# Kernel optimization log

Hardware: AMD Instinct MI355X
Metric: run time of the kernel (lower is better)

The kernel has to match this reference:

```python
import jax, jax.numpy as jnp
import numpy as np

# Dims fixed by ExpertC.__init__ defaults
INPUT_DIM, HIDDEN, OUT_DIM, NLAYERS = 1024, 256, 256, 2
D_STATE, EXPAND, HEADDIM = 32, 2, 32
D_INNER = EXPAND * HIDDEN                      # 512
NHEADS = D_INNER // HEADDIM                    # 16
CONV_DIM = D_INNER + 2 * D_STATE               # 576 (x, B, C; ngroups=1)
D_IN_PROJ = 2 * D_INNER + 2 * D_STATE + NHEADS # 1104 (z, xBC, dt)
KCONV = 4
B, L = 16, 2048
EPS = 1e-5


def setup_inputs() -> dict:
    key = jax.random.key(0)
    ks = iter(jax.random.split(key, 40))
    rn = lambda shape, s: jax.random.normal(next(ks), shape, jnp.float32) * s
    inp = {}
    inp["x"] = rn((B, L, INPUT_DIM), 1.0)
    inp["ip_w"] = rn((INPUT_DIM, HIDDEN), INPUT_DIM ** -0.5)
    inp["ip_b"] = jnp.zeros((HIDDEN,), jnp.float32)
    inp["m_inw"] = rn((NLAYERS, HIDDEN, D_IN_PROJ), HIDDEN ** -0.5)
    inp["m_inb"] = jnp.zeros((NLAYERS, D_IN_PROJ), jnp.float32)
    inp["m_convw"] = rn((NLAYERS, CONV_DIM, KCONV), 0.3)
    inp["m_convb"] = jnp.zeros((NLAYERS, CONV_DIM), jnp.float32)
    inp["m_dtb"] = rn((NLAYERS, NHEADS), 0.5)
    inp["m_Alog"] = jnp.log(1.0 + 15.0 * jax.random.uniform(next(ks), (NLAYERS, NHEADS), jnp.float32))
    inp["m_D"] = jnp.ones((NLAYERS, NHEADS), jnp.float32)
    inp["m_nw"] = jnp.ones((NLAYERS, D_INNER), jnp.float32)
    inp["m_outw"] = rn((NLAYERS, D_INNER, HIDDEN), D_INNER ** -0.5)
    inp["m_outb"] = jnp.zeros((NLAYERS, HIDDEN), jnp.float32)
    inp["rms_w"] = jnp.ones((NLAYERS, HIDDEN), jnp.float32)
    inp["ln1_w"] = jnp.ones((HIDDEN,), jnp.float32)
    inp["ln1_b"] = jnp.zeros((HIDDEN,), jnp.float32)
    inp["w1"] = rn((HIDDEN, 2 * HIDDEN), HIDDEN ** -0.5)
    inp["b1"] = jnp.zeros((2 * HIDDEN,), jnp.float32)
    inp["w2"] = rn((2 * HIDDEN, OUT_DIM), (2 * HIDDEN) ** -0.5)
    inp["b2"] = jnp.zeros((OUT_DIM,), jnp.float32)
    inp["ln2_w"] = jnp.ones((OUT_DIM,), jnp.float32)
    inp["ln2_b"] = jnp.zeros((OUT_DIM,), jnp.float32)
    return inp


def rmsnorm(x, w):
    return x * jax.lax.rsqrt(jnp.mean(x * x, axis=-1, keepdims=True) + EPS) * w


def layernorm(x, w, b):
    m = jnp.mean(x, axis=-1, keepdims=True)
    v = jnp.mean((x - m) ** 2, axis=-1, keepdims=True)
    return (x - m) * jax.lax.rsqrt(v + EPS) * w + b


def mamba_layer(x, inw, inb, convw, convb, dtb, Alog, D, nw, outw, outb):
    b, l, _ = x.shape
    zxbcdt = x @ inw + inb                                   # (b,l,1104)
    z, xBC, dt = jnp.split(zxbcdt, [D_INNER, D_INNER + CONV_DIM], axis=-1)
    dt = jax.nn.softplus(dt + dtb)                           # (b,l,h)
    # causal depthwise conv1d (kernel 4) + silu
    xp = jnp.pad(xBC, ((0, 0), (KCONV - 1, 0), (0, 0)))
    xBC = sum(xp[:, i:i + l, :] * convw[:, i] for i in range(KCONV)) + convb
    xBC = jax.nn.silu(xBC)
    xs, Bm, Cm = jnp.split(xBC, [D_INNER, D_INNER + D_STATE], axis=-1)
    xh = xs.reshape(b, l, NHEADS, HEADDIM)                   # (b,l,h,p)
    A = -jnp.exp(Alog)                                       # (h,)
    dA = jnp.exp(dt * A)                                     # (b,l,h)
    dtx = dt[..., None] * xh                                 # (b,l,h,p)

    def step(h, inp):
        dA_t, dtx_t, B_t, C_t = inp
        # h: (b,h,p,n)
        h = h * dA_t[:, :, None, None] + dtx_t[..., None] * B_t[:, None, None, :]
        y = jnp.einsum('bhpn,bn->bhp', h, C_t)
        return h, y

    h0 = jnp.zeros((b, NHEADS, HEADDIM, D_STATE), x.dtype)
    xs_t = (jnp.moveaxis(dA, 1, 0), jnp.moveaxis(dtx, 1, 0),
            jnp.moveaxis(Bm, 1, 0), jnp.moveaxis(Cm, 1, 0))
    _, ys = jax.lax.scan(step, h0, xs_t)                     # (l,b,h,p)
    y = jnp.moveaxis(ys, 0, 1) + D[None, None, :, None] * xh
    y = y.reshape(b, l, D_INNER)
    y = rmsnorm(y * jax.nn.silu(z), nw)                      # gated RMSNorm
    return y @ outw + outb


def _expert(x, ip_w, ip_b, m_inw, m_inb, m_convw, m_convb, m_dtb, m_Alog, m_D,
            m_nw, m_outw, m_outb, rms_w, ln1_w, ln1_b, w1, b1, w2, b2, ln2_w, ln2_b):
    if x.ndim == 2:
        x = x[:, None, :]
    x = x @ ip_w + ip_b
    for i in range(NLAYERS):
        res = x
        x = mamba_layer(x, m_inw[i], m_inb[i], m_convw[i], m_convb[i], m_dtb[i],
                        m_Alog[i], m_D[i], m_nw[i], m_outw[i], m_outb[i])
        x = rmsnorm(x + res, rms_w[i])
    x = layernorm(x, ln1_w, ln1_b)
    x = jax.nn.gelu(x @ w1 + b1, approximate=False)          # dropout is eval no-op
    x = x @ w2 + b2
    return layernorm(x, ln2_w, ln2_b)


def reference(x, ip_w, ip_b, m_inw, m_inb, m_convw, m_convb, m_dtb, m_Alog, m_D,
              m_nw, m_outw, m_outb, rms_w, ln1_w, ln1_b, w1, b1, w2, b2, ln2_w, ln2_b):
    return _expert(x, ip_w, ip_b, m_inw, m_inb, m_convw, m_convb, m_dtb, m_Alog, m_D,
                   m_nw, m_outw, m_outb, rms_w, ln1_w, ln1_b, w1, b1, w2, b2, ln2_w, ln2_b)
```

## Files before the change

kernel.cpp:

```cpp
#include <hip/hip_runtime.h>

typedef __bf16 bf16;
typedef __bf16 bf16x8 __attribute__((ext_vector_type(8)));
typedef float  f32x4  __attribute__((ext_vector_type(4)));

#define EPSF 1e-5f

__device__ __forceinline__ float bf2f(bf16 x) { return (float)x; }
__device__ __forceinline__ bf16  f2bf(float x) { return (bf16)x; }
__device__ __forceinline__ float siluf(float x) { return x / (1.f + expf(-x)); }

struct PrepackArgs {
    const float* W[7];
    bf16* TH[7];
    bf16* TL[7];
    int K[7];
    int N[7];
};

__global__ __launch_bounds__(256) void prepack_kernel(PrepackArgs a)
{
    int s = blockIdx.y;
    int idx = blockIdx.x * 256 + threadIdx.x;
    int K = a.K[s], N = a.N[s];
    if (idx >= K * N) return;
    int k = idx / N, n = idx - k * N;
    float v = a.W[s][idx];
    bf16 hi = f2bf(v);
    a.TH[s][(size_t)n * K + k] = hi;
    a.TL[s][(size_t)n * K + k] = f2bf(v - bf2f(hi));
}

__global__ __launch_bounds__(256) void gemm_hl(
    const bf16* __restrict__ AH, const bf16* __restrict__ AL,
    const float* __restrict__ Af, int lda,
    const bf16* __restrict__ WTh, const bf16* __restrict__ WTl,
    const float* __restrict__ bias,
    int N, int K,
    float* __restrict__ outF, int ldF,
    bf16* __restrict__ outB, int ldB,
    bf16* __restrict__ outH, bf16* __restrict__ outL, int ldH,
    int doGelu,
    const float* __restrict__ dtb, const float* __restrict__ Alog,
    float* __restrict__ dtf, float* __restrict__ dAf)
{
    __shared__ bf16 As [128][40];
    __shared__ bf16 Als[128][40];

    const int tid  = threadIdx.x;
    const int lane = tid & 63;
    const int wid  = tid >> 6;
    const int waveM = wid & 1, waveN = wid >> 1;
    const int m16 = lane & 15, quad = lane >> 4;
    const int row0 = blockIdx.x * 128;
    const int n0   = blockIdx.y * 64;

    f32x4 acc[4][2];
#pragma unroll
    for (int i = 0; i < 4; ++i)
#pragma unroll
        for (int j = 0; j < 2; ++j)
            acc[i][j] = (f32x4){0.f, 0.f, 0.f, 0.f};

    const int ar = tid >> 1, akc = (tid & 1) * 16;

    const int bn0 = min(n0 + waveN * 32 + m16,      N - 1);
    const int bn1 = min(n0 + waveN * 32 + 16 + m16, N - 1);
    const bf16* bH0p = WTh + (size_t)bn0 * K + quad * 8;
    const bf16* bH1p = WTh + (size_t)bn1 * K + quad * 8;
    const bf16* bL0p = WTl + (size_t)bn0 * K + quad * 8;
    const bf16* bL1p = WTl + (size_t)bn1 * K + quad * 8;

    bf16x8 bH[2], bL[2], bHn[2], bLn[2];
    bH[0] = *(const bf16x8*)(bH0p);
    bH[1] = *(const bf16x8*)(bH1p);
    bL[0] = *(const bf16x8*)(bL0p);
    bL[1] = *(const bf16x8*)(bL1p);

    for (int k0 = 0; k0 < K; k0 += 32) {
        if (AH) {
            const bf16* s0 = AH + (size_t)(row0 + ar) * lda + k0 + akc;
            const bf16* s1 = AL + (size_t)(row0 + ar) * lda + k0 + akc;
            *(uint4*)&As [ar][akc]     = *(const uint4*)s0;
            *(uint4*)&As [ar][akc + 8] = *(const uint4*)(s0 + 8);
            *(uint4*)&Als[ar][akc]     = *(const uint4*)s1;
            *(uint4*)&Als[ar][akc + 8] = *(const uint4*)(s1 + 8);
        } else {
            const float* asrc = Af + (size_t)(row0 + ar) * lda + k0 + akc;
            float f[16];
            *(float4*)&f[0]  = ((const float4*)asrc)[0];
            *(float4*)&f[4]  = ((const float4*)asrc)[1];
            *(float4*)&f[8]  = ((const float4*)asrc)[2];
            *(float4*)&f[12] = ((const float4*)asrc)[3];
            bf16 hv[16], lv[16];
#pragma unroll
            for (int c = 0; c < 16; ++c) {
                bf16 hi = f2bf(f[c]);
                hv[c] = hi;
                lv[c] = f2bf(f[c] - bf2f(hi));
            }
            *(uint4*)&As [ar][akc]     = *(uint4*)&hv[0];
            *(uint4*)&As [ar][akc + 8] = *(uint4*)&hv[8];
            *(uint4*)&Als[ar][akc]     = *(uint4*)&lv[0];
            *(uint4*)&Als[ar][akc + 8] = *(uint4*)&lv[8];
        }
        __syncthreads();

        const bool more = (k0 + 32) < K;
        if (more) {
            int kn = k0 + 32;
            bHn[0] = *(const bf16x8*)(bH0p + kn);
            bHn[1] = *(const bf16x8*)(bH1p + kn);
            bLn[0] = *(const bf16x8*)(bL0p + kn);
            bLn[1] = *(const bf16x8*)(bL1p + kn);
        }

        bf16x8 aH[4], aL[4];
#pragma unroll
        for (int mi = 0; mi < 4; ++mi) {
            aH[mi] = *(const bf16x8*)&As [waveM * 64 + mi * 16 + m16][quad * 8];
            aL[mi] = *(const bf16x8*)&Als[waveM * 64 + mi * 16 + m16][quad * 8];
        }

#pragma unroll
        for (int mi = 0; mi < 4; ++mi)
#pragma unroll
            for (int ni = 0; ni < 2; ++ni) {
                acc[mi][ni] = __builtin_amdgcn_mfma_f32_16x16x32_bf16(
                    aH[mi], bH[ni], acc[mi][ni], 0, 0, 0);
                acc[mi][ni] = __builtin_amdgcn_mfma_f32_16x16x32_bf16(
                    aH[mi], bL[ni], acc[mi][ni], 0, 0, 0);
                acc[mi][ni] = __builtin_amdgcn_mfma_f32_16x16x32_bf16(
                    aL[mi], bH[ni], acc[mi][ni], 0, 0, 0);
            }
        __syncthreads();

        if (more) {
            bH[0] = bHn[0]; bH[1] = bHn[1];
            bL[0] = bLn[0]; bL[1] = bLn[1];
        }
    }

#pragma unroll
    for (int ni = 0; ni < 2; ++ni) {
        int col = n0 + waveN * 32 + ni * 16 + m16;
        if (col >= N) continue;
        float bv = bias ? bias[col] : 0.f;
#pragma unroll
        for (int mi = 0; mi < 4; ++mi) {
#pragma unroll
            for (int r = 0; r < 4; ++r) {
                int row = row0 + waveM * 64 + mi * 16 + quad * 4 + r;
                float v = acc[mi][ni][r] + bv;
                if (dtf && col >= 1088) {
                    int head = col - 1088;
                    float xx = v + dtb[head];
                    float sp = (xx > 20.f) ? xx : log1pf(expf(xx));
                    float A  = -expf(Alog[head]);
                    dtf[(size_t)row * 16 + head] = sp;
                    dAf[(size_t)row * 16 + head] = expf(sp * A);
                } else {
                    if (doGelu) v = 0.5f * v * (1.f + erff(v * 0.70710678118654752f));
                    if (outB) outB[(size_t)row * ldB + col] = f2bf(v);
                    if (outF) outF[(size_t)row * ldF + col] = v;
                    if (outH) {
                        bf16 hi = f2bf(v);
                        outH[(size_t)row * ldH + col] = hi;
                        outL[(size_t)row * ldH + col] = f2bf(v - bf2f(hi));
                    }
                }
            }
        }
    }
}

__global__ __launch_bounds__(256) void conv_kernel(
    const bf16* __restrict__ zx,
    const float* __restrict__ cw,
    const float* __restrict__ cbias,
    float* __restrict__ xs,
    float* __restrict__ Bc,
    float* __restrict__ Cc)
{
    int g = blockIdx.x * 256 + threadIdx.x;
    if (g >= 32768 * 72) return;
    int row = g / 72;
    int cb8 = g - row * 72;
    int ch  = cb8 * 8;
    int l   = row & 2047;

    float4 wv[8];
#pragma unroll
    for (int c = 0; c < 8; ++c)
        wv[c] = *(const float4*)(cw + (ch + c) * 4);

    float acc[8];
    {
        float4 b0 = *(const float4*)(cbias + ch);
        float4 b1 = *(const float4*)(cbias + ch + 4);
        acc[0] = b0.x; acc[1] = b0.y; acc[2] = b0.z; acc[3] = b0.w;
        acc[4] = b1.x; acc[5] = b1.y; acc[6] = b1.z; acc[7] = b1.w;
    }

#pragma unroll
    for (int i = 0; i < 4; ++i) {
        int ls = l + i - 3;
        if (ls >= 0) {
            bf16x8 v = *(const bf16x8*)(zx + (size_t)(row + i - 3) * 1104 + 512 + ch);
#pragma unroll
            for (int c = 0; c < 8; ++c)
                acc[c] = fmaf(bf2f(v[c]), (&wv[c].x)[i], acc[c]);
        }
    }

    float s[8];
#pragma unroll
    for (int c = 0; c < 8; ++c) s[c] = siluf(acc[c]);

    if (cb8 < 64) {
        float* dst = xs + (size_t)row * 512 + ch;
        ((float4*)dst)[0] = (float4){s[0], s[1], s[2], s[3]};
        ((float4*)dst)[1] = (float4){s[4], s[5], s[6], s[7]};
    } else if (cb8 < 68) {
        float* dst = Bc + (size_t)row * 32 + (ch - 512);
        ((float4*)dst)[0] = (float4){s[0], s[1], s[2], s[3]};
        ((float4*)dst)[1] = (float4){s[4], s[5], s[6], s[7]};
    } else {
        float* dst = Cc + (size_t)row * 32 + (ch - 544);
        ((float4*)dst)[0] = (float4){s[0], s[1], s[2], s[3]};
        ((float4*)dst)[1] = (float4){s[4], s[5], s[6], s[7]};
    }
}

#define QCH   64
#define NCH   32

struct StepB  { float Bv[16]; float da, dtv, xv; };
struct StepBC { float Bv[16]; float Cv[16]; float da, dtv, xv; };

__device__ __forceinline__ void load_stepB(
    StepB& S, const float* Bc, const float* dtf, const float* dAf,
    const float* xs, size_t r, int h, int p, int nb)
{
    const float4* bp = (const float4*)(Bc + r * 32 + nb);
    *(float4*)&S.Bv[0]  = bp[0];
    *(float4*)&S.Bv[4]  = bp[1];
    *(float4*)&S.Bv[8]  = bp[2];
    *(float4*)&S.Bv[12] = bp[3];
    S.da  = dAf[r * 16 + h];
    S.dtv = dtf[r * 16 + h];
    S.xv  = xs[r * 512 + h * 32 + p];
}

__device__ __forceinline__ void load_stepBC(
    StepBC& S, const float* Bc, const float* Cc, const float* dtf,
    const float* dAf, const float* xs, size_t r, int h, int p, int nb)
{
    const float4* bp = (const float4*)(Bc + r * 32 + nb);
    *(float4*)&S.Bv[0]  = bp[0];
    *(float4*)&S.Bv[4]  = bp[1];
    *(float4*)&S.Bv[8]  = bp[2];
    *(float4*)&S.Bv[12] = bp[3];
    const float4* cp = (const float4*)(Cc + r * 32 + nb);
    *(float4*)&S.Cv[0]  = cp[0];
    *(float4*)&S.Cv[4]  = cp[1];
    *(float4*)&S.Cv[8]  = cp[2];
    *(float4*)&S.Cv[12] = cp[3];
    S.da  = dAf[r * 16 + h];
    S.dtv = dtf[r * 16 + h];
    S.xv  = xs[r * 512 + h * 32 + p];
}

__global__ __launch_bounds__(256) void scan_phase1(
    const float* __restrict__ xs,
    const float* __restrict__ Bc,
    const float* __restrict__ dtf,
    const float* __restrict__ dAf,
    float* __restrict__ cs,
    float* __restrict__ cp)
{
    int blk = blockIdx.x * 4 + (threadIdx.x >> 6);
    int bh = blk >> 5, c = blk & (NCH - 1);
    int b = bh >> 4, h = bh & 15;
    int lane = threadIdx.x & 63;
    int p = lane & 31, half = lane >> 5, nb = half * 16;
    float hs[16];
#pragma unroll
    for (int j = 0; j < 16; ++j) hs[j] = 0.f;
    float P = 1.f;
    size_t rb = (size_t)b * 2048 + (size_t)c * QCH;

    StepB S0, S1;
    load_stepB(S0, Bc, dtf, dAf, xs, rb, h, p, nb);

    for (int t = 0; t < QCH; t += 2) {
        load_stepB(S1, Bc, dtf, dAf, xs, rb + t + 1, h, p, nb);
        {
            float dtx = S0.dtv * S0.xv, da = S0.da;
#pragma unroll
            for (int j = 0; j < 16; ++j)
                hs[j] = fmaf(hs[j], da, dtx * S0.Bv[j]);
            P *= da;
        }
        if (t + 2 < QCH)
            load_stepB(S0, Bc, dtf, dAf, xs, rb + t + 2, h, p, nb);
        {
            float dtx = S1.dtv * S1.xv, da = S1.da;
#pragma unroll
            for (int j = 0; j < 16; ++j)
                hs[j] = fmaf(hs[j], da, dtx * S1.Bv[j]);
            P *= da;
        }
    }

    float* dst = cs + (size_t)blk * 1024 + lane * 16;
#pragma unroll
    for (int q = 0; q < 4; ++q)
        ((float4*)dst)[q] = (float4){hs[q*4], hs[q*4+1], hs[q*4+2], hs[q*4+3]};
    if (lane == 0) cp[blk] = P;
}

__global__ __launch_bounds__(64) void scan_phase2(
    float* __restrict__ cs,
    const float* __restrict__ cp)
{
    int bh = blockIdx.x;
    int lane = threadIdx.x;
    float H[16];
#pragma unroll
    for (int j = 0; j < 16; ++j) H[j] = 0.f;
    for (int c = 0; c < NCH; ++c) {
        float* base = cs + ((size_t)(bh * NCH + c)) * 1024 + lane * 16;
        float E[16];
#pragma unroll
        for (int q = 0; q < 4; ++q) {
            float4 v = ((const float4*)base)[q];
            E[q*4] = v.x; E[q*4+1] = v.y; E[q*4+2] = v.z; E[q*4+3] = v.w;
        }
        float P = cp[bh * NCH + c];
#pragma unroll
        for (int q = 0; q < 4; ++q)
            ((float4*)base)[q] = (float4){H[q*4], H[q*4+1], H[q*4+2], H[q*4+3]};
#pragma unroll
        for (int j = 0; j < 16; ++j)
            H[j] = fmaf(H[j], P, E[j]);
    }
}

__global__ __launch_bounds__(256) void scan_phase3(
    const float* __restrict__ xs,
    const float* __restrict__ Bc,
    const float* __restrict__ Cc,
    const float* __restrict__ dtf,
    const float* __restrict__ dAf,
    const float* __restrict__ Dv,
    const float* __restrict__ cs,
    bf16* __restrict__ zx)
{
    int blk = blockIdx.x * 4 + (threadIdx.x >> 6);
    int bh = blk >> 5, c = blk & (NCH - 1);
    int b = bh >> 4, h = bh & 15;
    int lane = threadIdx.x & 63;
    int p = lane & 31, half = lane >> 5, nb = half * 16;
    float Dh = Dv[h];
    float hs[16];
    {
        const float* src = cs + (size_t)blk * 1024 + lane * 16;
#pragma unroll
        for (int q = 0; q < 4; ++q) {
            float4 v = ((const float4*)src)[q];
            hs[q*4] = v.x; hs[q*4+1] = v.y; hs[q*4+2] = v.z; hs[q*4+3] = v.w;
        }
    }
    size_t rb = (size_t)b * 2048 + (size_t)c * QCH;

    StepBC S0, S1;
    load_stepBC(S0, Bc, Cc, dtf, dAf, xs, rb, h, p, nb);

    for (int t = 0; t < QCH; t += 2) {
        load_stepBC(S1, Bc, Cc, dtf, dAf, xs, rb + t + 1, h, p, nb);
        {
            float dtx = S0.dtv * S0.xv, da = S0.da;
            float y0 = 0.f, y1 = 0.f, y2 = 0.f, y3 = 0.f;
#pragma unroll
            for (int j = 0; j < 16; j += 4) {
                hs[j]   = fmaf(hs[j],   da, dtx * S0.Bv[j]);   y0 = fmaf(hs[j],   S0.Cv[j],   y0);
                hs[j+1] = fmaf(hs[j+1], da, dtx * S0.Bv[j+1]); y1 = fmaf(hs[j+1], S0.Cv[j+1], y1);
                hs[j+2] = fmaf(hs[j+2], da, dtx * S0.Bv[j+2]); y2 = fmaf(hs[j+2], S0.Cv[j+2], y2);
                hs[j+3] = fmaf(hs[j+3], da, dtx * S0.Bv[j+3]); y3 = fmaf(hs[j+3], S0.Cv[j+3], y3);
            }
            float yv = (y0 + y1) + (y2 + y3);
            yv += __shfl_xor(yv, 32);
            if (half == 0)
                zx[(rb + t) * 1104 + 512 + h * 32 + p] = f2bf(yv + Dh * S0.xv);
        }
        if (t + 2 < QCH)
            load_stepBC(S0, Bc, Cc, dtf, dAf, xs, rb + t + 2, h, p, nb);
        {
            float dtx = S1.dtv * S1.xv, da = S1.da;
            float y0 = 0.f, y1 = 0.f, y2 = 0.f, y3 = 0.f;
#pragma unroll
            for (int j = 0; j < 16; j += 4) {
                hs[j]   = fmaf(hs[j],   da, dtx * S1.Bv[j]);   y0 = fmaf(hs[j],   S1.Cv[j],   y0);
                hs[j+1] = fmaf(hs[j+1], da, dtx * S1.Bv[j+1]); y1 = fmaf(hs[j+1], S1.Cv[j+1], y1);
                hs[j+2] = fmaf(hs[j+2], da, dtx * S1.Bv[j+2]); y2 = fmaf(hs[j+2], S1.Cv[j+2], y2);
                hs[j+3] = fmaf(hs[j+3], da, dtx * S1.Bv[j+3]); y3 = fmaf(hs[j+3], S1.Cv[j+3], y3);
            }
            float yv = (y0 + y1) + (y2 + y3);
            yv += __shfl_xor(yv, 32);
            if (half == 0)
                zx[(rb + t + 1) * 1104 + 512 + h * 32 + p] = f2bf(yv + Dh * S1.xv);
        }
    }
}

__global__ __launch_bounds__(256) void gaterms_kernel(
    const bf16* __restrict__ zx,
    const float* __restrict__ nw,
    bf16* __restrict__ outH,
    bf16* __restrict__ outL)
{
    int row = blockIdx.x * 4 + (threadIdx.x >> 6);
    int lane = threadIdx.x & 63;
    union { uint4 u; bf16 b[8]; } yv, zv, oh, ol;
    yv.u = *(const uint4*)(zx + (size_t)row * 1104 + 512 + lane * 8);
    zv.u = *(const uint4*)(zx + (size_t)row * 1104 + lane * 8);
    float4 nv0 = *(const float4*)(nw + lane * 8);
    float4 nv1 = *(const float4*)(nw + lane * 8 + 4);
    float nvv[8] = {nv0.x, nv0.y, nv0.z, nv0.w, nv1.x, nv1.y, nv1.z, nv1.w};
    float g[8]; float ss = 0.f;
#pragma unroll
    for (int i = 0; i < 8; ++i) {
        float gate = siluf(bf2f(zv.b[i]));
        g[i] = bf2f(yv.b[i]) * gate;
        ss += g[i] * g[i];
    }
#pragma unroll
    for (int o = 1; o < 64; o <<= 1) ss += __shfl_xor(ss, o);
    float rms = rsqrtf(ss * (1.f / 512.f) + EPSF);
#pragma unroll
    for (int i = 0; i < 8; ++i) {
        float v = g[i] * rms * nvv[i];
        bf16 hi = f2bf(v);
        oh.b[i] = hi;
        ol.b[i] = f2bf(v - bf2f(hi));
    }
    *(uint4*)(outH + (size_t)row * 512 + lane * 8) = oh.u;
    *(uint4*)(outL + (size_t)row * 512 + lane * 8) = ol.u;
}

__global__ __launch_bounds__(256) void resrms_kernel(
    const float* __restrict__ mo,
    float* __restrict__ h,
    const float* __restrict__ w,
    bf16* __restrict__ oH,
    bf16* __restrict__ oL)
{
    int row = blockIdx.x * 4 + (threadIdx.x >> 6);
    int lane = threadIdx.x & 63;
    float4 a = *(const float4*)(mo + (size_t)row * 256 + lane * 4);
    float4 r = *(const float4*)(h  + (size_t)row * 256 + lane * 4);
    float s0 = a.x + r.x, s1 = a.y + r.y, s2 = a.z + r.z, s3 = a.w + r.w;
    float ss = s0 * s0 + s1 * s1 + s2 * s2 + s3 * s3;
#pragma unroll
    for (int o = 1; o < 64; o <<= 1) ss += __shfl_xor(ss, o);
    float rms = rsqrtf(ss * (1.f / 256.f) + EPSF);
    float4 wv = *(const float4*)(w + lane * 4);
    float o0 = s0 * rms * wv.x, o1 = s1 * rms * wv.y;
    float o2 = s2 * rms * wv.z, o3 = s3 * rms * wv.w;
    *(float4*)(h + (size_t)row * 256 + lane * 4) = (float4){o0, o1, o2, o3};
    union { uint2 u; bf16 bb[4]; } uh, ul;
    float o[4] = {o0, o1, o2, o3};
#pragma unroll
    for (int i = 0; i < 4; ++i) {
        bf16 hi = f2bf(o[i]);
        uh.bb[i] = hi;
        ul.bb[i] = f2bf(o[i] - bf2f(hi));
    }
    *(uint2*)(oH + (size_t)row * 256 + lane * 4) = uh.u;
    *(uint2*)(oL + (size_t)row * 256 + lane * 4) = ul.u;
}

__global__ __launch_bounds__(256) void ln_kernel(
    const float* __restrict__ x,
    const float* __restrict__ w,
    const float* __restrict__ b,
    bf16* __restrict__ outH,
    bf16* __restrict__ outL,
    float* __restrict__ outF)
{
    int row = blockIdx.x * 4 + (threadIdx.x >> 6);
    int lane = threadIdx.x & 63;
    float4 v = *(const float4*)(x + (size_t)row * 256 + lane * 4);
    float sum = v.x + v.y + v.z + v.w;
    float sq  = v.x * v.x + v.y * v.y + v.z * v.z + v.w * v.w;
#pragma unroll
    for (int o = 1; o < 64; o <<= 1) { sum += __shfl_xor(sum, o); sq += __shfl_xor(sq, o); }
    float m  = sum * (1.f / 256.f);
    float var = sq * (1.f / 256.f) - m * m;
    float is = rsqrtf(var + EPSF);
    float4 wv = *(const float4*)(w + lane * 4);
    float4 bv = *(const float4*)(b + lane * 4);
    float o0 = (v.x - m) * is * wv.x + bv.x;
    float o1 = (v.y - m) * is * wv.y + bv.y;
    float o2 = (v.z - m) * is * wv.z + bv.z;
    float o3 = (v.w - m) * is * wv.w + bv.w;
    if (outH) {
        union { uint2 u; bf16 bb[4]; } oh, ol;
        float o[4] = {o0, o1, o2, o3};
#pragma unroll
        for (int i = 0; i < 4; ++i) {
            bf16 hi = f2bf(o[i]);
            oh.bb[i] = hi;
            ol.bb[i] = f2bf(o[i] - bf2f(hi));
        }
        *(uint2*)(outH + (size_t)row * 256 + lane * 4) = oh.u;
        *(uint2*)(outL + (size_t)row * 256 + lane * 4) = ol.u;
    }
    if (outF)
        *(float4*)(outF + (size_t)row * 256 + lane * 4) = (float4){o0, o1, o2, o3};
}

extern "C" void kernel_launch(void* const* d_in, const int* in_sizes, int n_in,
                              void* d_out, int out_size, void* d_ws, size_t ws_size,
                              hipStream_t stream)
{
    const float* x      = (const float*)d_in[0];
    const float* ip_w   = (const float*)d_in[1];
    const float* ip_b   = (const float*)d_in[2];
    const float* m_inw  = (const float*)d_in[3];
    const float* m_inb  = (const float*)d_in[4];
    const float* m_convw= (const float*)d_in[5];
    const float* m_convb= (const float*)d_in[6];
    const float* m_dtb  = (const float*)d_in[7];
    const float* m_Alog = (const float*)d_in[8];
    const float* m_D    = (const float*)d_in[9];
    const float* m_nw   = (const float*)d_in[10];
    const float* m_outw = (const float*)d_in[11];
    const float* m_outb = (const float*)d_in[12];
    const float* rms_w  = (const float*)d_in[13];
    const float* ln1_w  = (const float*)d_in[14];
    const float* ln1_b  = (const float*)d_in[15];
    const float* w1     = (const float*)d_in[16];
    const float* b1     = (const float*)d_in[17];
    const float* w2     = (const float*)d_in[18];
    const float* b2     = (const float*)d_in[19];
    const float* ln2_w  = (const float*)d_in[20];
    const float* ln2_b  = (const float*)d_in[21];

    const int M = 32768;
    char* wsb = (char*)d_ws;
    size_t off = 0;
    auto alloc = [&](size_t bytes) {
        void* p = wsb + off;
        off += (bytes + 255) & ~(size_t)255;
        return p;
    };
    bf16*  zx   = (bf16*) alloc((size_t)M * 1104 * 2);
    float* h    = (float*)alloc((size_t)M * 256 * 4);
    float* U1   = (float*)alloc((size_t)M * 512 * 4);
    float* Bc   = (float*)alloc((size_t)M * 32 * 4);
    float* Cc   = (float*)alloc((size_t)M * 32 * 4);
    float* dtf  = (float*)alloc((size_t)M * 16 * 4);
    float* dAf  = (float*)alloc((size_t)M * 16 * 4);
    float* cs   = (float*)alloc((size_t)8192 * 1024 * 4);
    float* cpb  = (float*)alloc((size_t)8192 * 4);
    bf16* ipTH   = (bf16*)alloc(262144 * 2);
    bf16* ipTL   = (bf16*)alloc(262144 * 2);
    bf16* inwTH0 = (bf16*)alloc(282624 * 2);
    bf16* inwTL0 = (bf16*)alloc(282624 * 2);
    bf16* inwTH1 = (bf16*)alloc(282624 * 2);
    bf16* inwTL1 = (bf16*)alloc(282624 * 2);
    bf16* outwTH0= (bf16*)alloc(131072 * 2);
    bf16* outwTL0= (bf16*)alloc(131072 * 2);
    bf16* outwTH1= (bf16*)alloc(131072 * 2);
    bf16* outwTL1= (bf16*)alloc(131072 * 2);
    bf16* w1TH   = (bf16*)alloc(131072 * 2);
    bf16* w1TL   = (bf16*)alloc(131072 * 2);
    bf16* w2TH   = (bf16*)alloc(131072 * 2);
    bf16* w2TL   = (bf16*)alloc(131072 * 2);
    (void)ws_size; (void)in_sizes; (void)n_in; (void)out_size;

    float* xs      = U1;
    bf16*  hH      = (bf16*)U1;
    bf16*  hL      = hH + (size_t)M * 256;
    bf16*  normedH = (bf16*)U1;
    bf16*  normedL = normedH + (size_t)M * 512;
    bf16*  tbH     = (bf16*)U1;
    bf16*  tbL     = tbH + (size_t)M * 256;
    float* mo      = (float*)zx;
    bf16*  gH      = (bf16*)zx;
    bf16*  gL      = gH + (size_t)M * 512;
    float* ubuf    = (float*)cs;

    PrepackArgs pa;
    pa.W[0] = ip_w;               pa.TH[0] = ipTH;    pa.TL[0] = ipTL;    pa.K[0] = 1024; pa.N[0] = 256;
    pa.W[1] = m_inw;              pa.TH[1] = inwTH0;  pa.TL[1] = inwTL0;  pa.K[1] = 256;  pa.N[1] = 1104;
    pa.W[2] = m_inw + 256*1104;   pa.TH[2] = inwTH1;  pa.TL[2] = inwTL1;  pa.K[2] = 256;  pa.N[2] = 1104;
    pa.W[3] = m_outw;             pa.TH[3] = outwTH0; pa.TL[3] = outwTL0; pa.K[3] = 512;  pa.N[3] = 256;
    pa.W[4] = m_outw + 512*256;   pa.TH[4] = outwTH1; pa.TL[4] = outwTL1; pa.K[4] = 512;  pa.N[4] = 256;
    pa.W[5] = w1;                 pa.TH[5] = w1TH;    pa.TL[5] = w1TL;    pa.K[5] = 256;  pa.N[5] = 512;
    pa.W[6] = w2;                 pa.TH[6] = w2TH;    pa.TL[6] = w2TL;    pa.K[6] = 512;  pa.N[6] = 256;
    prepack_kernel<<<dim3(1104, 7), 256, 0, stream>>>(pa);

    dim3 blk(256);

    gemm_hl<<<dim3(256, 4), blk, 0, stream>>>(
        nullptr, nullptr, x, 1024, ipTH, ipTL, ip_b, 256, 1024,
        h, 256, nullptr, 0, hH, hL, 256, 0,
        nullptr, nullptr, nullptr, nullptr);

    for (int L = 0; L < 2; ++L) {
        const bf16* inwTH = L ? inwTH1 : inwTH0;
        const bf16* inwTL = L ? inwTL1 : inwTL0;
        const bf16* outwTH= L ? outwTH1 : outwTH0;
        const bf16* outwTL= L ? outwTL1 : outwTL0;
        const float* inb = m_inb  + (size_t)L * 1104;
        const float* cw  = m_convw+ (size_t)L * 576 * 4;
        const float* cb  = m_convb+ (size_t)L * 576;
        const float* dtb = m_dtb  + L * 16;
        const float* Al  = m_Alog + L * 16;
        const float* Dv  = m_D    + L * 16;
        const float* nw  = m_nw   + (size_t)L * 512;
        const float* ob  = m_outb + (size_t)L * 256;
        const float* rw  = rms_w  + (size_t)L * 256;

        gemm_hl<<<dim3(256, 18), blk, 0, stream>>>(
            hH, hL, nullptr, 256, inwTH, inwTL, inb, 1104, 256,
            nullptr, 0, zx, 1104, nullptr, nullptr, 0, 0,
            dtb, Al, dtf, dAf);
        conv_kernel<<<9216, 256, 0, stream>>>(zx, cw, cb, xs, Bc, Cc);
        scan_phase1<<<2048, 256, 0, stream>>>(xs, Bc, dtf, dAf, cs, cpb);
        scan_phase2<<<256, 64, 0, stream>>>(cs, cpb);
        scan_phase3<<<2048, 256, 0, stream>>>(xs, Bc, Cc, dtf, dAf, Dv, cs, zx);
        gaterms_kernel<<<M / 4, 256, 0, stream>>>(zx, nw, normedH, normedL);
        gemm_hl<<<dim3(256, 4), blk, 0, stream>>>(
            normedH, normedL, nullptr, 512, outwTH, outwTL, ob, 256, 512,
            mo, 256, nullptr, 0, nullptr, nullptr, 0, 0,
            nullptr, nullptr, nullptr, nullptr);
        resrms_kernel<<<M / 4, 256, 0, stream>>>(mo, h, rw, hH, hL);
    }

    ln_kernel<<<M / 4, 256, 0, stream>>>(h, ln1_w, ln1_b, tbH, tbL, nullptr);
    gemm_hl<<<dim3(256, 8), blk, 0, stream>>>(
        tbH, tbL, nullptr, 256, w1TH, w1TL, b1, 512, 256,
        nullptr, 0, nullptr, 0, gH, gL, 512, 1,
        nullptr, nullptr, nullptr, nullptr);
    gemm_hl<<<dim3(256, 4), blk, 0, stream>>>(
        gH, gL, nullptr, 512, w2TH, w2TL, b2, 256, 512,
        ubuf, 256, nullptr, 0, nullptr, nullptr, 0, 0,
        nullptr, nullptr, nullptr, nullptr);
    ln_kernel<<<M / 4, 256, 0, stream>>>(ubuf, ln2_w, ln2_b, nullptr, nullptr, (float*)d_out);
}
```

Measured before the change: 1.564 ms.

## Double-buffer A tile in LDS with XOR swizzle and register prefetch

The GEMM A-tile staging now uses two LDS buffers. The next k-slice is loaded from global into registers before the MFMA loop and written to the alternate buffer afterwards, so each iteration needs one barrier instead of two. The hi and lo halves are packed into a single 64-wide row with an XOR swizzle to avoid LDS bank conflicts. This adds register pressure for the prefetched values and doubles LDS use per block, which may lower occupancy.

```diff
diff --git a/kernel.cpp b/kernel.cpp
--- a/kernel.cpp
+++ b/kernel.cpp
@@ -44,8 +44,7 @@
     const float* __restrict__ dtb, const float* __restrict__ Alog,
     float* __restrict__ dtf, float* __restrict__ dAf)
 {
-    __shared__ bf16 As [128][40];
-    __shared__ bf16 Als[128][40];
+    __shared__ bf16 As[2][128][64];
 
     const int tid  = threadIdx.x;
     const int lane = tid & 63;
@@ -62,7 +61,18 @@
         for (int j = 0; j < 2; ++j)
             acc[i][j] = (f32x4){0.f, 0.f, 0.f, 0.f};
 
-    const int ar = tid >> 1, akc = (tid & 1) * 16;
+    const int ar  = tid >> 1;
+    const int akc = (tid & 1) * 16;
+    const int ac0 = (tid & 1) * 2;
+    const int sw  = ar & 7;
+    const int sH0 = ((ac0 + 0) ^ sw) * 8;
+    const int sH1 = ((ac0 + 1) ^ sw) * 8;
+    const int sL0 = ((ac0 + 4) ^ sw) * 8;
+    const int sL1 = ((ac0 + 5) ^ sw) * 8;
+
+    const int rs = m16 & 7;
+    const int rH = ((quad + 0) ^ rs) * 8;
+    const int rL = ((quad + 4) ^ rs) * 8;
 
     const int bn0 = min(n0 + waveN * 32 + m16,      N - 1);
     const int bn1 = min(n0 + waveN * 32 + 16 + m16, N - 1);
@@ -77,21 +87,38 @@
     bL[0] = *(const bf16x8*)(bL0p);
     bL[1] = *(const bf16x8*)(bL1p);
 
-    for (int k0 = 0; k0 < K; k0 += 32) {
+    uint4  pH0, pH1, pL0, pL1;
+    float4 fA0, fA1, fA2, fA3;
+
+    auto loadA = [&](int k0) {
         if (AH) {
             const bf16* s0 = AH + (size_t)(row0 + ar) * lda + k0 + akc;
             const bf16* s1 = AL + (size_t)(row0 + ar) * lda + k0 + akc;
-            *(uint4*)&As [ar][akc]     = *(const uint4*)s0;
-            *(uint4*)&As [ar][akc + 8] = *(const uint4*)(s0 + 8);
-            *(uint4*)&Als[ar][akc]     = *(const uint4*)s1;
-            *(uint4*)&Als[ar][akc + 8] = *(const uint4*)(s1 + 8);
+            pH0 = *(const uint4*)s0;
+            pH1 = *(const uint4*)(s0 + 8);
+            pL0 = *(const uint4*)s1;
+            pL1 = *(const uint4*)(s1 + 8);
         } else {
             const float* asrc = Af + (size_t)(row0 + ar) * lda + k0 + akc;
+            fA0 = ((const float4*)asrc)[0];
+            fA1 = ((const float4*)asrc)[1];
+            fA2 = ((const float4*)asrc)[2];
+            fA3 = ((const float4*)asrc)[3];
+        }
+    };
+    auto writeA = [&](int buf) {
+        bf16* dst = &As[buf][ar][0];
+        if (AH) {
+            *(uint4*)(dst + sH0) = pH0;
+            *(uint4*)(dst + sH1) = pH1;
+            *(uint4*)(dst + sL0) = pL0;
+            *(uint4*)(dst + sL1) = pL1;
+        } else {
             float f[16];
-            *(float4*)&f[0]  = ((const float4*)asrc)[0];
-            *(float4*)&f[4]  = ((const float4*)asrc)[1];
-            *(float4*)&f[8]  = ((const float4*)asrc)[2];
-            *(float4*)&f[12] = ((const float4*)asrc)[3];
+            *(float4*)&f[0]  = fA0;
+            *(float4*)&f[4]  = fA1;
+            *(float4*)&f[8]  = fA2;
+            *(float4*)&f[12] = fA3;
             bf16 hv[16], lv[16];
 #pragma unroll
             for (int c = 0; c < 16; ++c) {
@@ -99,15 +126,23 @@
                 hv[c] = hi;
                 lv[c] = f2bf(f[c] - bf2f(hi));
             }
-            *(uint4*)&As [ar][akc]     = *(uint4*)&hv[0];
-            *(uint4*)&As [ar][akc + 8] = *(uint4*)&hv[8];
-            *(uint4*)&Als[ar][akc]     = *(uint4*)&lv[0];
-            *(uint4*)&Als[ar][akc + 8] = *(uint4*)&lv[8];
-        }
-        __syncthreads();
-
+            *(uint4*)(dst + sH0) = *(uint4*)&hv[0];
+            *(uint4*)(dst + sH1) = *(uint4*)&hv[8];
+            *(uint4*)(dst + sL0) = *(uint4*)&lv[0];
+            *(uint4*)(dst + sL1) = *(uint4*)&lv[8];
+        }
+    };
+
+    loadA(0);
+    writeA(0);
+    __syncthreads();
+
+    int cur = 0;
+    for (int k0 = 0; k0 < K; k0 += 32) {
         const bool more = (k0 + 32) < K;
+
         if (more) {
+            loadA(k0 + 32);
             int kn = k0 + 32;
             bHn[0] = *(const bf16x8*)(bH0p + kn);
             bHn[1] = *(const bf16x8*)(bH1p + kn);
@@ -118,8 +153,9 @@
         bf16x8 aH[4], aL[4];
 #pragma unroll
         for (int mi = 0; mi < 4; ++mi) {
-            aH[mi] = *(const bf16x8*)&As [waveM * 64 + mi * 16 + m16][quad * 8];
-            aL[mi] = *(const bf16x8*)&Als[waveM * 64 + mi * 16 + m16][quad * 8];
+            const bf16* base = &As[cur][waveM * 64 + mi * 16 + m16][0];
+            aH[mi] = *(const bf16x8*)(base + rH);
+            aL[mi] = *(const bf16x8*)(base + rL);
         }
 
 #pragma unroll
@@ -133,12 +169,14 @@
                 acc[mi][ni] = __builtin_amdgcn_mfma_f32_16x16x32_bf16(
                     aL[mi], bH[ni], acc[mi][ni], 0, 0, 0);
             }
+
+        if (more) writeA(cur ^ 1);
         __syncthreads();
-
         if (more) {
             bH[0] = bHn[0]; bH[1] = bHn[1];
             bL[0] = bLn[0]; bL[1] = bLn[1];
         }
+        cur ^= 1;
     }
 
 #pragma unroll
```

New measurement: 1.769 ms. 1.13x slower.
